# Kernel tuning notes

Hardware: AMD Instinct MI355X
Metric: run time of the kernel (lower is better)

## Reference

```python
import math
import jax, jax.numpy as jnp
import numpy as np

EPS = 1e-4
FMAX = 18  # max filtersize for scale clamped to 2.5: ceil(3*2^2.5+0.5)=18 -> kernel 37x37
KSZ = 2 * FMAX + 1


def _conv2d(x, w, b):
    # 3x3 conv, padding 1, NCHW / OIHW (cross-correlation, matches torch)
    y = jax.lax.conv_general_dilated(x, w, (1, 1), [(1, 1), (1, 1)],
                                     dimension_numbers=('NCHW', 'OIHW', 'NCHW'))
    return y + b[None, :, None, None]


def _basis_filters(scale):
    # scale: [B] -> [B,3,K,K] (g, dgdx, dgdy), masked to the per-sample support
    std = 2.0 ** scale                              # [B]
    fs = jnp.ceil(3.0 * std + 0.5)                  # per-sample filtersize
    x = jnp.arange(-FMAX, FMAX + 1, dtype=jnp.float32)          # [K]
    m = (jnp.abs(x)[None, :] <= fs[:, None]).astype(jnp.float32)  # [B,K] support mask
    e = jnp.exp(-0.5 * (x[None, :] / std[:, None]) ** 2) * m      # masked 1D gaussian [B,K]
    g = e[:, :, None] * e[:, None, :]                              # [B,K,K]
    g = g / jnp.sum(g, axis=(1, 2), keepdims=True)
    c = (-x[None, :] / (std[:, None] ** 3 * 2.0 * math.pi)) * e    # [B,K]
    dgdx = c[:, :, None] * e[:, None, :]   # varies along first spatial dim (x[0])
    dgdx = dgdx / jnp.sum(jnp.abs(dgdx), axis=(1, 2), keepdims=True)
    dgdy = e[:, :, None] * c[:, None, :]   # varies along second spatial dim (x[1])
    dgdy = dgdy / jnp.sum(jnp.abs(dgdy), axis=(1, 2), keepdims=True)
    return jnp.stack([g, dgdx, dgdy], axis=1)  # [B,3,K,K]


def setup_inputs() -> dict:
    key = jax.random.key(0)
    ks = jax.random.split(key, 7)
    B, H, W = 8, 512, 512
    batch = jax.random.uniform(ks[0], (B, 3, H, W), dtype=jnp.float32)
    gcm = jnp.array([[0.06, 0.63, 0.27], [0.3, 0.04, -0.35], [0.34, -0.6, 0.17]],
                    dtype=jnp.float32)
    w1 = jax.random.normal(ks[1], (16, 3, 3, 3), dtype=jnp.float32) * 0.1
    b1 = jax.random.normal(ks[2], (16,), dtype=jnp.float32) * 0.01
    w2 = jax.random.normal(ks[3], (16, 16, 3, 3), dtype=jnp.float32) * 0.1
    b2 = jax.random.normal(ks[4], (16,), dtype=jnp.float32) * 0.01
    w3 = jax.random.normal(ks[5], (1, 16, 3, 3), dtype=jnp.float32) * 0.1
    b3 = jax.random.normal(ks[6], (1,), dtype=jnp.float32) * 0.01
    return {"batch": batch, "gcm": gcm, "w1": w1, "b1": b1,
            "w2": w2, "b2": b2, "w3": w3, "b3": b3}


def reference(batch, gcm, w1, b1, w2, b2, w3, b3):
    B, _, H, W = batch.shape
    # ---- RGB order prior (non-differentiable, no_grad in torch) ----
    oh = lambda i: jax.nn.one_hot(i, 3, axis=1, dtype=batch.dtype)
    mx = jnp.argmax(batch, axis=1)                 # first max
    mn = jnp.argmin(batch, axis=1)
    bf = batch[:, ::-1]
    mx2 = 2 - jnp.argmax(bf, axis=1)               # last max
    mn2 = 2 - jnp.argmin(bf, axis=1)
    RGB_order = jax.lax.stop_gradient(
        0.5 * (oh(mx) + oh(mx2)) - 0.5 * (oh(mn) + oh(mn2)))  # [B,3,H,W]

    # ---- per-sample adaptive scale from small CNN ----
    h = jax.nn.silu(_conv2d(batch, w1, b1))
    h = jax.nn.silu(_conv2d(h, w2, b2))
    s = _conv2d(h, w3, b3)
    scale = jnp.clip(jnp.mean(s, axis=(1, 2, 3)), -2.5, 2.5)   # [B]

    # ---- Gaussian color model ----
    xg = jnp.einsum('ij,bjhw->bihw', gcm, batch)  # [B,3,H,W] -> (E, El, Ell)

    # ---- per-sample Gaussian basis convolution, batched via grouped conv ----
    basis = _basis_filters(scale)                                  # [B,3,K,K]
    xin = xg.reshape(1, B * 3, H, W)
    wk = jnp.broadcast_to(basis[:, None], (B, 3, 3, KSZ, KSZ)).reshape(B * 9, 1, KSZ, KSZ)
    out = jax.lax.conv_general_dilated(xin, wk, (1, 1), [(FMAX, FMAX), (FMAX, FMAX)],
                                       feature_group_count=B * 3,
                                       dimension_numbers=('NCHW', 'OIHW', 'NCHW'))
    out = out.reshape(B, 3, 3, H, W)   # [B, chan(E/El/Ell), filt(g/dx/dy), H, W]
    E = out[:, 0, 0:1]
    Ex = out[:, 0, 1:2]
    Ey = out[:, 0, 2:3]
    El = out[:, 1, 0:1]
    Ell = out[:, 2, 0:1]

    Hf = jnp.arctan(El / (Ell + EPS))
    S = jnp.log((El ** 2 + Ell ** 2) / (E ** 2 + EPS) + EPS)
    Ww = jnp.arctan((Ex / (E + EPS)) ** 2 + (Ey / (E + EPS)) ** 2)
    return jnp.concatenate([Hf, S, RGB_order, Ww], axis=1)  # [B,6,H,W]
```

## Files before the change

kernel.cpp:

```cpp
#include <hip/hip_runtime.h>
#include <hip/hip_bf16.h>

constexpr int BN = 8, HH = 512, WW = 512;
constexpr int PIX = HH * WW;
constexpr float EPSF = 1e-4f;

__device__ __forceinline__ float b2f(__hip_bfloat16 x) { return __bfloat162float(x); }
__device__ __forceinline__ __hip_bfloat16 f2b(float x) { return __float2bfloat16(x); }
__device__ __forceinline__ unsigned short bfbits(float x) {
    union { __hip_bfloat16 b; unsigned short u; } cv; cv.b = f2b(x); return cv.u;
}

typedef __attribute__((ext_vector_type(8))) short bf16x8;
typedef __attribute__((ext_vector_type(4))) float f32x4;

constexpr int OFF_TOT = 0;
constexpr int OFF_ROW0 = 128;
constexpr int OFF_ROW1 = 256;
constexpr int OFF_COL0 = 384;
constexpr int OFF_COL1 = 512;
constexpr int OFF_COR = 640;
constexpr int OFF_WR  = 2048;
constexpr int OFF_EH  = 4608;
constexpr int OFF_CH  = 5120;
constexpr size_t OFF_XGB = 65536;
constexpr size_t XG_BYTES = (size_t)BN * 3 * PIX * 4;
constexpr size_t OFF_TPB = OFF_XGB + XG_BYTES;
constexpr size_t TP_BYTES = (size_t)4 * BN * PIX * 4;
constexpr size_t WS_NEEDED = OFF_TPB + TP_BYTES;

__global__ void prep_kernel(const float* __restrict__ w2, float* __restrict__ wsf) {
    int t = threadIdx.x;
    for (int i = t; i < 640; i += 256) wsf[i] = 0.f;
    unsigned short* ab = (unsigned short*)(wsf + OFF_WR);
    for (int idx = t; idx < 5120; idx += 256) {
        int part = idx / 2560;
        int id = idx - part * 2560;
        int ks = id >> 9, rem = id & 511, lane = rem >> 3, j = id & 7;
        int oc = lane & 15, q = lane >> 4;
        int k = q * 8 + j;
        int tap = 2 * ks + (k >> 4), ic = k & 15;
        float val = (tap <= 8) ? w2[oc * 144 + ic * 9 + tap] : 0.f;
        float hv = b2f(f2b(val));
        ab[idx] = (part == 0) ? bfbits(val) : bfbits(val - hv);
    }
}

__global__ __launch_bounds__(256) void conv12_kernel(const float* __restrict__ batch,
                                                     const float* __restrict__ w1,
                                                     const float* __restrict__ b1,
                                                     const unsigned short* __restrict__ abuf,
                                                     const float* __restrict__ b2v,
                                                     const float* __restrict__ gcm,
                                                     float* __restrict__ wsf,
                                                     float* __restrict__ xg,
                                                     float* __restrict__ out) {
    __shared__ uint4 h1s[18 * 66 * 2];
    __shared__ float part[4][16];

    int tx = threadIdx.x;
    int lane = tx & 63, wave = tx >> 6;
    int n = lane & 15, q = lane >> 4;
    int w0 = blockIdx.x * 64, h0 = blockIdx.y * 16, b = blockIdx.z;

    union { uint4 u; bf16x8 v; } cv;
    bf16x8 ah[5], al[5];
    const uint4* ab4 = (const uint4*)abuf;
#pragma unroll
    for (int ks = 0; ks < 5; ks++) {
        cv.u = ab4[ks * 64 + lane];       ah[ks] = cv.v;
        cv.u = ab4[320 + ks * 64 + lane]; al[ks] = cv.v;
    }

    const float* pb = batch + (size_t)(b * 3) * PIX;
    for (int i = tx; i < 18 * 66; i += 256) {
        int r = i / 66, c = i - r * 66;
        int gh = h0 - 1 + r, gw = w0 - 1 + c;
        unsigned int u[8];
        if (gh >= 0 && gh < HH && gw >= 0 && gw < WW) {
            float v[27];
#pragma unroll
            for (int ic = 0; ic < 3; ic++) {
                const float* p = pb + (size_t)ic * PIX;
#pragma unroll
                for (int kh = 0; kh < 3; kh++) {
                    int hh = gh + kh - 1;
#pragma unroll
                    for (int kw = 0; kw < 3; kw++) {
                        int ww = gw + kw - 1;
                        float x = 0.f;
                        if (hh >= 0 && hh < HH && ww >= 0 && ww < WW) x = p[hh * WW + ww];
                        v[ic * 9 + kh * 3 + kw] = x;
                    }
                }
            }
            float o[16];
#pragma unroll
            for (int oc = 0; oc < 16; oc++) {
                float a = b1[oc];
#pragma unroll
                for (int j = 0; j < 27; j++) a += v[j] * w1[oc * 27 + j];
                o[oc] = a / (1.f + __expf(-a));
            }
#pragma unroll
            for (int k = 0; k < 8; k++)
                u[k] = (unsigned int)bfbits(o[2 * k]) | ((unsigned int)bfbits(o[2 * k + 1]) << 16);
        } else {
#pragma unroll
            for (int k = 0; k < 8; k++) u[k] = 0u;
        }
        int swz = (c >> 2) & 1;
        int base = i * 2;
        h1s[base + swz]       = make_uint4(u[0], u[1], u[2], u[3]);
        h1s[base + (swz ^ 1)] = make_uint4(u[4], u[5], u[6], u[7]);
    }

    for (int j = tx; j < 1024; j += 256) {
        int rr = j >> 6, ccx = j & 63;
        int gh = h0 + rr, gw = w0 + ccx;
        size_t p = (size_t)gh * WW + gw;
        float v0 = pb[p], v1 = pb[(size_t)PIX + p], v2 = pb[2 * (size_t)PIX + p];
#pragma unroll
        for (int i = 0; i < 3; i++)
            xg[(size_t)(b * 3 + i) * PIX + p] =
                gcm[i * 3] * v0 + gcm[i * 3 + 1] * v1 + gcm[i * 3 + 2] * v2;
        int mx  = (v0 >= v1 && v0 >= v2) ? 0 : ((v1 >= v2) ? 1 : 2);
        int mx2 = (v2 >= v1 && v2 >= v0) ? 2 : ((v1 >= v0) ? 1 : 0);
        int mn  = (v0 <= v1 && v0 <= v2) ? 0 : ((v1 <= v2) ? 1 : 2);
        int mn2 = (v2 <= v1 && v2 <= v0) ? 2 : ((v1 <= v0) ? 1 : 0);
#pragma unroll
        for (int c = 0; c < 3; c++) {
            float r = 0.5f * ((float)(c == mx) + (float)(c == mx2))
                    - 0.5f * ((float)(c == mn) + (float)(c == mn2));
            out[(size_t)(b * 6 + 2 + c) * PIX + p] = r;
        }
    }
    __syncthreads();

    float tt[4] = {0, 0, 0, 0};
    float cs0[4] = {0, 0, 0, 0};
    float cs1[4] = {0, 0, 0, 0};
    for (int rloc = 0; rloc < 4; rloc++) {
        int row = wave * 4 + rloc;
        int grow = h0 + row;
        f32x4 acc[4] = {{0,0,0,0},{0,0,0,0},{0,0,0,0},{0,0,0,0}};
#pragma unroll
        for (int ks = 0; ks < 5; ks++) {
            int tap = 2 * ks + (q >> 1); if (tap > 8) tap = 8;
            int dh = tap / 3 - 1, dw = tap % 3 - 1;
            int half = q & 1;
            int lr = row + 1 + dh;
#pragma unroll
            for (int t = 0; t < 4; t++) {
                int c = 1 + dw + t * 16 + n;
                cv.u = h1s[(lr * 66 + c) * 2 + (half ^ ((c >> 2) & 1))];
                acc[t] = __builtin_amdgcn_mfma_f32_16x16x32_bf16(ah[ks], cv.v, acc[t], 0, 0, 0);
                acc[t] = __builtin_amdgcn_mfma_f32_16x16x32_bf16(al[ks], cv.v, acc[t], 0, 0, 0);
            }
        }
        float sv[4][4];
#pragma unroll
        for (int t = 0; t < 4; t++)
#pragma unroll
            for (int r = 0; r < 4; r++) {
                float a = acc[t][r] + b2v[q * 4 + r];
                sv[t][r] = a / (1.f + __expf(-a));
            }
#pragma unroll
        for (int r = 0; r < 4; r++) tt[r] += sv[0][r] + sv[1][r] + sv[2][r] + sv[3][r];
        if (grow == 0 || grow == HH - 1) {
            int off = (grow == 0) ? OFF_ROW0 : OFF_ROW1;
#pragma unroll
            for (int r = 0; r < 4; r++) {
                float x = sv[0][r] + sv[1][r] + sv[2][r] + sv[3][r];
#pragma unroll
                for (int d = 1; d < 16; d <<= 1) x += __shfl_xor(x, d, 64);
                if (n == 0) atomicAdd(&wsf[off + b * 16 + q * 4 + r], x);
            }
        }
        if (blockIdx.x == 0 && n == 0)
#pragma unroll
            for (int r = 0; r < 4; r++) cs0[r] += sv[0][r];
        if (blockIdx.x == 7 && n == 15)
#pragma unroll
            for (int r = 0; r < 4; r++) cs1[r] += sv[3][r];
        if ((grow == 0 || grow == HH - 1)) {
            int hi = (grow == 0) ? 0 : 1;
            if (blockIdx.x == 0 && n == 0)
#pragma unroll
                for (int r = 0; r < 4; r++)
                    wsf[OFF_COR + ((b * 2 + hi) * 2 + 0) * 16 + q * 4 + r] = sv[0][r];
            if (blockIdx.x == 7 && n == 15)
#pragma unroll
                for (int r = 0; r < 4; r++)
                    wsf[OFF_COR + ((b * 2 + hi) * 2 + 1) * 16 + q * 4 + r] = sv[3][r];
        }
    }
    if (blockIdx.x == 0 && n == 0)
#pragma unroll
        for (int r = 0; r < 4; r++) atomicAdd(&wsf[OFF_COL0 + b * 16 + q * 4 + r], cs0[r]);
    if (blockIdx.x == 7 && n == 15)
#pragma unroll
        for (int r = 0; r < 4; r++) atomicAdd(&wsf[OFF_COL1 + b * 16 + q * 4 + r], cs1[r]);
#pragma unroll
    for (int r = 0; r < 4; r++) {
        float x = tt[r];
#pragma unroll
        for (int d = 1; d < 16; d <<= 1) x += __shfl_xor(x, d, 64);
        tt[r] = x;
    }
    if (n == 0)
#pragma unroll
        for (int r = 0; r < 4; r++) part[wave][q * 4 + r] = tt[r];
    __syncthreads();
    if (tx < 16)
        atomicAdd(&wsf[OFF_TOT + b * 16 + tx],
                  part[0][tx] + part[1][tx] + part[2][tx] + part[3][tx]);
}

__global__ void filter_kernel(const float* __restrict__ w3, const float* __restrict__ b3,
                              float* __restrict__ wsf) {
    int b = blockIdx.x, t = threadIdx.x;
    __shared__ float red[160];
    float val = 0.f;
    if (t < 144) {
        int ic = t / 9, tap = t % 9, kh = tap / 3, kw = tap % 3;
        float T = wsf[OFF_TOT + b * 16 + ic];
        int hi = -1, wi = -1;
        if (kh == 0) { T -= wsf[OFF_ROW1 + b * 16 + ic]; hi = 1; }
        else if (kh == 2) { T -= wsf[OFF_ROW0 + b * 16 + ic]; hi = 0; }
        if (kw == 0) { T -= wsf[OFF_COL1 + b * 16 + ic]; wi = 1; }
        else if (kw == 2) { T -= wsf[OFF_COL0 + b * 16 + ic]; wi = 0; }
        if (hi >= 0 && wi >= 0) T += wsf[OFF_COR + ((b * 2 + hi) * 2 + wi) * 16 + ic];
        val = w3[t] * T;
    }
    red[t] = val;
    __syncthreads();
    __shared__ float sh_mean;
    if (t == 0) {
        float S = 0.f;
        for (int i = 0; i < 144; i++) S += red[i];
        sh_mean = b3[0] + S * (1.f / (float)PIX);
    }
    __syncthreads();
    float scale = fminf(2.5f, fmaxf(-2.5f, sh_mean));
    float sd = exp2f(scale);
    float fs = ceilf(3.f * sd + 0.5f);
    float e = 0.f, c = 0.f;
    if (t < 37) {
        float x = (float)(t - 18);
        if (fabsf(x) <= fs) {
            float qq = x / sd;
            e = __expf(-0.5f * qq * qq);
            c = -x / (sd * sd * sd * 6.28318530717958647692f) * e;
        }
    }
    __shared__ float sa[40], sb[40];
    if (t < 37) { sa[t] = e; sb[t] = fabsf(c); }
    __syncthreads();
    __shared__ float Se, Sc;
    if (t == 0) {
        float a = 0.f, d = 0.f;
        for (int i = 0; i < 37; i++) { a += sa[i]; d += sb[i]; }
        Se = a; Sc = d;
    }
    __syncthreads();
    if (t < 37) {
        wsf[OFF_EH + b * 37 + t] = e / Se;
        wsf[OFF_CH + b * 37 + t] = c / Sc;
    }
}

__global__ __launch_bounds__(256) void horiz_kernel(const float* __restrict__ xg,
                                                    const float* __restrict__ ehat,
                                                    const float* __restrict__ chat,
                                                    float* __restrict__ t) {
    __shared__ float L[3][296];
    int tid = threadIdx.x;
    int w0 = blockIdx.x * 256;
    int h = blockIdx.y;
    int b = blockIdx.z;
    for (int i = tid; i < 3 * 292; i += 256) {
        int c = i / 292, j = i - c * 292;
        int gw = w0 - 18 + j;
        float x = 0.f;
        if (gw >= 0 && gw < WW) x = xg[(size_t)(b * 3 + c) * PIX + h * WW + gw];
        L[c][j] = x;
    }
    __syncthreads();
    const float* eh = ehat + b * 37; const float* ch = chat + b * 37;
    float s0e = 0.f, s0c = 0.f, s1e = 0.f, s2e = 0.f;
    for (int k = 0; k < 37; k++) {
        float ce = eh[k], cc = ch[k];
        float a0 = L[0][tid + k], a1 = L[1][tid + k], a2 = L[2][tid + k];
        s0e += ce * a0; s0c += cc * a0; s1e += ce * a1; s2e += ce * a2;
    }
    int w = w0 + tid;
    size_t p = (size_t)b * PIX + h * WW + w;
    const size_t PL = (size_t)BN * PIX;
    t[0 * PL + p] = s0e;
    t[1 * PL + p] = s1e;
    t[2 * PL + p] = s2e;
    t[3 * PL + p] = s0c;
}

__global__ __launch_bounds__(256) void vert_kernel(const float* __restrict__ t,
                                                   const float* __restrict__ ehat,
                                                   const float* __restrict__ chat,
                                                   float* __restrict__ out) {
    int tx = threadIdx.x, ty = threadIdx.y;
    int w4 = (blockIdx.x * 64 + tx) * 4;
    int b = blockIdx.z;
    int h0 = (blockIdx.y * 4 + ty) * 4;
    const float* eh = ehat + b * 37; const float* ch = chat + b * 37;
    const size_t PL = (size_t)BN * PIX;
    const float* t0 = t + 0 * PL + (size_t)b * PIX;
    const float* t1 = t + 1 * PL + (size_t)b * PIX;
    const float* t2 = t + 2 * PL + (size_t)b * PIX;
    const float* t3 = t + 3 * PL + (size_t)b * PIX;
    float E[4][4] = {}, Ex[4][4] = {}, Ey[4][4] = {}, El[4][4] = {}, Ell[4][4] = {};
    for (int jj = 0; jj < 40; jj++) {
        int j = h0 - 18 + jj;
        if (j < 0 || j >= HH) continue;
        size_t idx = (size_t)j * WW + w4;
        float4 a0 = *(const float4*)(t0 + idx);
        float4 a1 = *(const float4*)(t1 + idx);
        float4 a2 = *(const float4*)(t2 + idx);
        float4 a3 = *(const float4*)(t3 + idx);
        float c0[4] = {a0.x, a0.y, a0.z, a0.w};
        float c1[4] = {a1.x, a1.y, a1.z, a1.w};
        float c2[4] = {a2.x, a2.y, a2.z, a2.w};
        float c3[4] = {a3.x, a3.y, a3.z, a3.w};
#pragma unroll
        for (int i = 0; i < 4; i++) {
            int k = jj - i;
            if (k >= 0 && k < 37) {
                float ce = eh[k], cc = ch[k];
#pragma unroll
                for (int x = 0; x < 4; x++) {
                    E[i][x] += ce * c0[x]; Ex[i][x] += cc * c0[x]; Ey[i][x] += ce * c3[x];
                    El[i][x] += ce * c1[x]; Ell[i][x] += ce * c2[x];
                }
            }
        }
    }
#pragma unroll
    for (int i = 0; i < 4; i++) {
        int h = h0 + i;
        float4 oH, oS, oW;
        float* pH = (float*)&oH; float* pS = (float*)&oS; float* pW = (float*)&oW;
#pragma unroll
        for (int x = 0; x < 4; x++) {
            pH[x] = atanf(El[i][x] / (Ell[i][x] + EPSF));
            pS[x] = logf((El[i][x] * El[i][x] + Ell[i][x] * Ell[i][x])
                         / (E[i][x] * E[i][x] + EPSF) + EPSF);
            float rx = Ex[i][x] / (E[i][x] + EPSF), ry = Ey[i][x] / (E[i][x] + EPSF);
            pW[x] = atanf(rx * rx + ry * ry);
        }
        size_t base = (size_t)(b * 6) * PIX + (size_t)h * WW + w4;
        *(float4*)(out + base) = oH;
        *(float4*)(out + base + PIX) = oS;
        *(float4*)(out + base + 5 * (size_t)PIX) = oW;
    }
}

extern "C" void kernel_launch(void* const* d_in, const int* in_sizes, int n_in,
                              void* d_out, int out_size, void* d_ws, size_t ws_size,
                              hipStream_t stream) {
    const float* batch = (const float*)d_in[0];
    const float* gcm   = (const float*)d_in[1];
    const float* w1    = (const float*)d_in[2];
    const float* b1    = (const float*)d_in[3];
    const float* w2    = (const float*)d_in[4];
    const float* b2    = (const float*)d_in[5];
    const float* w3    = (const float*)d_in[6];
    const float* b3    = (const float*)d_in[7];
    float* out = (float*)d_out;

    if (ws_size < WS_NEEDED) return;

    float* wsf = (float*)d_ws;
    float* xg  = (float*)((char*)d_ws + OFF_XGB);
    float* tpl = (float*)((char*)d_ws + OFF_TPB);
    float* ehat = wsf + OFF_EH;
    float* chat = wsf + OFF_CH;

    prep_kernel<<<dim3(1), dim3(256), 0, stream>>>(w2, wsf);
    conv12_kernel<<<dim3(8, 32, 8), dim3(256), 0, stream>>>(
        batch, w1, b1, (const unsigned short*)(wsf + OFF_WR), b2, gcm, wsf, xg, out);
    filter_kernel<<<dim3(8), dim3(160), 0, stream>>>(w3, b3, wsf);
    horiz_kernel<<<dim3(2, 512, 8), dim3(256), 0, stream>>>(xg, ehat, chat, tpl);
    vert_kernel<<<dim3(2, 32, 8), dim3(64, 4), 0, stream>>>(tpl, ehat, chat, out);
}
```

Baseline: 255.3 us.

## Fuse color model into horizontal pass, add interior fast path, retile separable filters

Stops writing the intermediate xg color-model tensor from the conv kernel and instead recomputes the 3x3 color transform from the input batch inside the horizontal filter kernel, cutting a full-size write and reread. Adds a branch-free interior path for the first conv's neighbourhood loads on non-edge blocks. The horizontal pass now handles 4 rows per block with 8 outputs per thread via register blocking from shared memory. The vertical pass switches to one column per thread with 8 rows each and scalar coalesced accesses. The cost is more redundant batch reads in the horizontal kernel and heavier per-thread register use.

```diff
diff --git a/kernel.cpp b/kernel.cpp
--- a/kernel.cpp
+++ b/kernel.cpp
@@ -23,9 +23,7 @@
 constexpr int OFF_WR  = 2048;
 constexpr int OFF_EH  = 4608;
 constexpr int OFF_CH  = 5120;
-constexpr size_t OFF_XGB = 65536;
-constexpr size_t XG_BYTES = (size_t)BN * 3 * PIX * 4;
-constexpr size_t OFF_TPB = OFF_XGB + XG_BYTES;
+constexpr size_t OFF_TPB = 65536;
 constexpr size_t TP_BYTES = (size_t)4 * BN * PIX * 4;
 constexpr size_t WS_NEEDED = OFF_TPB + TP_BYTES;
 
@@ -46,6 +44,21 @@
     }
 }
 
+__device__ __forceinline__ void conv1_px(const float v[27], const float* __restrict__ w1,
+                                         const float* __restrict__ b1, unsigned int u[8]) {
+    float o[16];
+#pragma unroll
+    for (int oc = 0; oc < 16; oc++) {
+        float a = b1[oc];
+#pragma unroll
+        for (int j = 0; j < 27; j++) a += v[j] * w1[oc * 27 + j];
+        o[oc] = a / (1.f + __expf(-a));
+    }
+#pragma unroll
+    for (int k = 0; k < 8; k++)
+        u[k] = (unsigned int)bfbits(o[2 * k]) | ((unsigned int)bfbits(o[2 * k + 1]) << 16);
+}
+
 __global__ __launch_bounds__(256) void conv12_kernel(const float* __restrict__ batch,
                                                      const float* __restrict__ w1,
                                                      const float* __restrict__ b1,
@@ -53,7 +66,6 @@
                                                      const float* __restrict__ b2v,
                                                      const float* __restrict__ gcm,
                                                      float* __restrict__ wsf,
-                                                     float* __restrict__ xg,
                                                      float* __restrict__ out) {
     __shared__ uint4 h1s[18 * 66 * 2];
     __shared__ float part[4][16];
@@ -62,6 +74,7 @@
     int lane = tx & 63, wave = tx >> 6;
     int n = lane & 15, q = lane >> 4;
     int w0 = blockIdx.x * 64, h0 = blockIdx.y * 16, b = blockIdx.z;
+    bool edge = (blockIdx.x == 0) || (blockIdx.x == 7) || (blockIdx.y == 0) || (blockIdx.y == 31);
 
     union { uint4 u; bf16x8 v; } cv;
     bf16x8 ah[5], al[5];
@@ -77,7 +90,18 @@
         int r = i / 66, c = i - r * 66;
         int gh = h0 - 1 + r, gw = w0 - 1 + c;
         unsigned int u[8];
-        if (gh >= 0 && gh < HH && gw >= 0 && gw < WW) {
+        if (!edge) {
+            const float* p0 = pb + (size_t)(gh - 1) * WW + (gw - 1);
+            float v[27];
+#pragma unroll
+            for (int ic = 0; ic < 3; ic++)
+#pragma unroll
+                for (int kh = 0; kh < 3; kh++)
+#pragma unroll
+                    for (int kw = 0; kw < 3; kw++)
+                        v[ic * 9 + kh * 3 + kw] = p0[(size_t)ic * PIX + kh * WW + kw];
+            conv1_px(v, w1, b1, u);
+        } else if (gh >= 0 && gh < HH && gw >= 0 && gw < WW) {
             float v[27];
 #pragma unroll
             for (int ic = 0; ic < 3; ic++) {
@@ -94,17 +118,7 @@
                     }
                 }
             }
-            float o[16];
-#pragma unroll
-            for (int oc = 0; oc < 16; oc++) {
-                float a = b1[oc];
-#pragma unroll
-                for (int j = 0; j < 27; j++) a += v[j] * w1[oc * 27 + j];
-                o[oc] = a / (1.f + __expf(-a));
-            }
-#pragma unroll
-            for (int k = 0; k < 8; k++)
-                u[k] = (unsigned int)bfbits(o[2 * k]) | ((unsigned int)bfbits(o[2 * k + 1]) << 16);
+            conv1_px(v, w1, b1, u);
         } else {
 #pragma unroll
             for (int k = 0; k < 8; k++) u[k] = 0u;
@@ -117,13 +131,8 @@
 
     for (int j = tx; j < 1024; j += 256) {
         int rr = j >> 6, ccx = j & 63;
-        int gh = h0 + rr, gw = w0 + ccx;
-        size_t p = (size_t)gh * WW + gw;
+        size_t p = (size_t)(h0 + rr) * WW + (w0 + ccx);
         float v0 = pb[p], v1 = pb[(size_t)PIX + p], v2 = pb[2 * (size_t)PIX + p];
-#pragma unroll
-        for (int i = 0; i < 3; i++)
-            xg[(size_t)(b * 3 + i) * PIX + p] =
-                gcm[i * 3] * v0 + gcm[i * 3 + 1] * v1 + gcm[i * 3 + 2] * v2;
         int mx  = (v0 >= v1 && v0 >= v2) ? 0 : ((v1 >= v2) ? 1 : 2);
         int mx2 = (v2 >= v1 && v2 >= v0) ? 2 : ((v1 >= v0) ? 1 : 0);
         int mn  = (v0 <= v1 && v0 <= v2) ? 0 : ((v1 <= v2) ? 1 : 2);
@@ -271,96 +280,109 @@
     }
 }
 
-__global__ __launch_bounds__(256) void horiz_kernel(const float* __restrict__ xg,
+__global__ __launch_bounds__(256) void horiz_kernel(const float* __restrict__ batch,
+                                                    const float* __restrict__ gcm,
                                                     const float* __restrict__ ehat,
                                                     const float* __restrict__ chat,
                                                     float* __restrict__ t) {
-    __shared__ float L[3][296];
-    int tid = threadIdx.x;
-    int w0 = blockIdx.x * 256;
-    int h = blockIdx.y;
-    int b = blockIdx.z;
-    for (int i = tid; i < 3 * 292; i += 256) {
-        int c = i / 292, j = i - c * 292;
-        int gw = w0 - 18 + j;
-        float x = 0.f;
-        if (gw >= 0 && gw < WW) x = xg[(size_t)(b * 3 + c) * PIX + h * WW + gw];
-        L[c][j] = x;
-    }
-    __syncthreads();
+    __shared__ float xr[4][3][556];
+    int tx = threadIdx.x;
+    int h0 = blockIdx.x * 4;
+    int b  = blockIdx.y;
+    const float* pb = batch + (size_t)(b * 3) * PIX;
+    float g0 = gcm[0], g1 = gcm[1], g2 = gcm[2];
+    float g3 = gcm[3], g4 = gcm[4], g5 = gcm[5];
+    float g6 = gcm[6], g7 = gcm[7], g8 = gcm[8];
+    for (int i = tx; i < 4 * 548; i += 256) {
+        int r = i / 548, c = i - r * 548;
+        int gw = c - 18;
+        float v0 = 0.f, v1 = 0.f, v2 = 0.f;
+        if (gw >= 0 && gw < WW) {
+            size_t p = (size_t)(h0 + r) * WW + gw;
+            v0 = pb[p]; v1 = pb[(size_t)PIX + p]; v2 = pb[2 * (size_t)PIX + p];
+        }
+        xr[r][0][c] = g0 * v0 + g1 * v1 + g2 * v2;
+        xr[r][1][c] = g3 * v0 + g4 * v1 + g5 * v2;
+        xr[r][2][c] = g6 * v0 + g7 * v1 + g8 * v2;
+    }
+    __syncthreads();
+    int r = tx >> 6, colbase = (tx & 63) * 8;
     const float* eh = ehat + b * 37; const float* ch = chat + b * 37;
-    float s0e = 0.f, s0c = 0.f, s1e = 0.f, s2e = 0.f;
-    for (int k = 0; k < 37; k++) {
-        float ce = eh[k], cc = ch[k];
-        float a0 = L[0][tid + k], a1 = L[1][tid + k], a2 = L[2][tid + k];
-        s0e += ce * a0; s0c += cc * a0; s1e += ce * a1; s2e += ce * a2;
-    }
-    int w = w0 + tid;
-    size_t p = (size_t)b * PIX + h * WW + w;
+    float a0[8] = {}, a1[8] = {}, a2[8] = {}, a3[8] = {};
+#pragma unroll
+    for (int k4 = 0; k4 < 11; k4++) {
+        float4 x0 = *(const float4*)&xr[r][0][colbase + k4 * 4];
+        float4 x1 = *(const float4*)&xr[r][1][colbase + k4 * 4];
+        float4 x2 = *(const float4*)&xr[r][2][colbase + k4 * 4];
+        const float* s0 = (const float*)&x0;
+        const float* s1 = (const float*)&x1;
+        const float* s2 = (const float*)&x2;
+#pragma unroll
+        for (int s = 0; s < 4; s++) {
+            int kk = k4 * 4 + s;
+#pragma unroll
+            for (int i = 0; i < 8; i++) {
+                int k = kk - i;
+                if (k >= 0 && k < 37) {
+                    float ce = eh[k], cc = ch[k];
+                    a0[i] += ce * s0[s]; a1[i] += ce * s1[s];
+                    a2[i] += ce * s2[s]; a3[i] += cc * s0[s];
+                }
+            }
+        }
+    }
     const size_t PL = (size_t)BN * PIX;
-    t[0 * PL + p] = s0e;
-    t[1 * PL + p] = s1e;
-    t[2 * PL + p] = s2e;
-    t[3 * PL + p] = s0c;
+    size_t p = (size_t)b * PIX + (size_t)(h0 + r) * WW + colbase;
+    *(float4*)&t[0 * PL + p]     = make_float4(a0[0], a0[1], a0[2], a0[3]);
+    *(float4*)&t[0 * PL + p + 4] = make_float4(a0[4], a0[5], a0[6], a0[7]);
+    *(float4*)&t[1 * PL + p]     = make_float4(a1[0], a1[1], a1[2], a1[3]);
+    *(float4*)&t[1 * PL + p + 4] = make_float4(a1[4], a1[5], a1[6], a1[7]);
+    *(float4*)&t[2 * PL + p]     = make_float4(a2[0], a2[1], a2[2], a2[3]);
+    *(float4*)&t[2 * PL + p + 4] = make_float4(a2[4], a2[5], a2[6], a2[7]);
+    *(float4*)&t[3 * PL + p]     = make_float4(a3[0], a3[1], a3[2], a3[3]);
+    *(float4*)&t[3 * PL + p + 4] = make_float4(a3[4], a3[5], a3[6], a3[7]);
 }
 
 __global__ __launch_bounds__(256) void vert_kernel(const float* __restrict__ t,
                                                    const float* __restrict__ ehat,
                                                    const float* __restrict__ chat,
                                                    float* __restrict__ out) {
-    int tx = threadIdx.x, ty = threadIdx.y;
-    int w4 = (blockIdx.x * 64 + tx) * 4;
+    int tx = threadIdx.x;
+    int j = blockIdx.x * 64 + (tx & 63);
+    int r0 = blockIdx.y * 32 + (tx >> 6) * 8;
     int b = blockIdx.z;
-    int h0 = (blockIdx.y * 4 + ty) * 4;
     const float* eh = ehat + b * 37; const float* ch = chat + b * 37;
     const size_t PL = (size_t)BN * PIX;
-    const float* t0 = t + 0 * PL + (size_t)b * PIX;
-    const float* t1 = t + 1 * PL + (size_t)b * PIX;
-    const float* t2 = t + 2 * PL + (size_t)b * PIX;
-    const float* t3 = t + 3 * PL + (size_t)b * PIX;
-    float E[4][4] = {}, Ex[4][4] = {}, Ey[4][4] = {}, El[4][4] = {}, Ell[4][4] = {};
-    for (int jj = 0; jj < 40; jj++) {
-        int j = h0 - 18 + jj;
-        if (j < 0 || j >= HH) continue;
-        size_t idx = (size_t)j * WW + w4;
-        float4 a0 = *(const float4*)(t0 + idx);
-        float4 a1 = *(const float4*)(t1 + idx);
-        float4 a2 = *(const float4*)(t2 + idx);
-        float4 a3 = *(const float4*)(t3 + idx);
-        float c0[4] = {a0.x, a0.y, a0.z, a0.w};
-        float c1[4] = {a1.x, a1.y, a1.z, a1.w};
-        float c2[4] = {a2.x, a2.y, a2.z, a2.w};
-        float c3[4] = {a3.x, a3.y, a3.z, a3.w};
-#pragma unroll
-        for (int i = 0; i < 4; i++) {
-            int k = jj - i;
-            if (k >= 0 && k < 37) {
-                float ce = eh[k], cc = ch[k];
-#pragma unroll
-                for (int x = 0; x < 4; x++) {
-                    E[i][x] += ce * c0[x]; Ex[i][x] += cc * c0[x]; Ey[i][x] += ce * c3[x];
-                    El[i][x] += ce * c1[x]; Ell[i][x] += ce * c2[x];
+    const float* t0 = t + (size_t)b * PIX;
+    float E[8] = {}, Ex[8] = {}, Ey[8] = {}, El[8] = {}, Ell[8] = {};
+#pragma unroll
+    for (int kk = 0; kk < 44; kk++) {
+        int gr = r0 - 18 + kk;
+        if (gr >= 0 && gr < HH) {
+            size_t idx = (size_t)gr * WW + j;
+            float v0 = t0[idx], v1 = t0[PL + idx], v2 = t0[2 * PL + idx], v3 = t0[3 * PL + idx];
+#pragma unroll
+            for (int i = 0; i < 8; i++) {
+                int k = kk - i;
+                if (k >= 0 && k < 37) {
+                    float ce = eh[k], cc = ch[k];
+                    E[i] += ce * v0; Ex[i] += cc * v0; Ey[i] += ce * v3;
+                    El[i] += ce * v1; Ell[i] += ce * v2;
                 }
             }
         }
     }
 #pragma unroll
-    for (int i = 0; i < 4; i++) {
-        int h = h0 + i;
-        float4 oH, oS, oW;
-        float* pH = (float*)&oH; float* pS = (float*)&oS; float* pW = (float*)&oW;
-#pragma unroll
-        for (int x = 0; x < 4; x++) {
-            pH[x] = atanf(El[i][x] / (Ell[i][x] + EPSF));
-            pS[x] = logf((El[i][x] * El[i][x] + Ell[i][x] * Ell[i][x])
-                         / (E[i][x] * E[i][x] + EPSF) + EPSF);
-            float rx = Ex[i][x] / (E[i][x] + EPSF), ry = Ey[i][x] / (E[i][x] + EPSF);
-            pW[x] = atanf(rx * rx + ry * ry);
-        }
-        size_t base = (size_t)(b * 6) * PIX + (size_t)h * WW + w4;
-        *(float4*)(out + base) = oH;
-        *(float4*)(out + base + PIX) = oS;
-        *(float4*)(out + base + 5 * (size_t)PIX) = oW;
+    for (int i = 0; i < 8; i++) {
+        int h = r0 + i;
+        float Hf = atanf(El[i] / (Ell[i] + EPSF));
+        float S = logf((El[i] * El[i] + Ell[i] * Ell[i]) / (E[i] * E[i] + EPSF) + EPSF);
+        float rx = Ex[i] / (E[i] + EPSF), ry = Ey[i] / (E[i] + EPSF);
+        float Wv = atanf(rx * rx + ry * ry);
+        size_t base = (size_t)(b * 6) * PIX + (size_t)h * WW + j;
+        out[base] = Hf;
+        out[base + PIX] = S;
+        out[base + 5 * (size_t)PIX] = Wv;
     }
 }
 
@@ -380,15 +402,14 @@
     if (ws_size < WS_NEEDED) return;
 
     float* wsf = (float*)d_ws;
-    float* xg  = (float*)((char*)d_ws + OFF_XGB);
     float* tpl = (float*)((char*)d_ws + OFF_TPB);
     float* ehat = wsf + OFF_EH;
     float* chat = wsf + OFF_CH;
 
     prep_kernel<<<dim3(1), dim3(256), 0, stream>>>(w2, wsf);
     conv12_kernel<<<dim3(8, 32, 8), dim3(256), 0, stream>>>(
-        batch, w1, b1, (const unsigned short*)(wsf + OFF_WR), b2, gcm, wsf, xg, out);
+        batch, w1, b1, (const unsigned short*)(wsf + OFF_WR), b2, gcm, wsf, out);
     filter_kernel<<<dim3(8), dim3(160), 0, stream>>>(w3, b3, wsf);
-    horiz_kernel<<<dim3(2, 512, 8), dim3(256), 0, stream>>>(xg, ehat, chat, tpl);
-    vert_kernel<<<dim3(2, 32, 8), dim3(64, 4), 0, stream>>>(tpl, ehat, chat, out);
-}
+    horiz_kernel<<<dim3(128, 8), dim3(256), 0, stream>>>(batch, gcm, ehat, chat, tpl);
+    vert_kernel<<<dim3(8, 16, 8), dim3(256), 0, stream>>>(tpl, ehat, chat, out);
+}
```

Measured after the change: 269.6 us. 1.06x slower.
